# Performance work log

Hardware: AMD Instinct MI355X
Metric: run time of the kernel (lower is better)

## Reference

```python
import jax, jax.numpy as jnp
import numpy as np

N_LEAVES = 4096
NF = N_LEAVES            # one-hot leaf feature dim
NN = 2 * N_LEAVES - 1    # nodes in binary backbone tree
HID = 512
T_MIN, T_MAX = 0.0, 1.0  # time_grid endpoints


def _belief_prop(node_sample, ch0, ch1, parent):
    """Postorder c/d recursion then preorder correction, as in node_embedding_site_backbone.
    Node ids are topologically ordered (children < parent), so postorder = 0..NN-1."""
    is_leaf = node_sample >= 0
    leaf_d = jax.nn.one_hot(jnp.clip(node_sample, 0), NF, dtype=jnp.float32)
    c0 = jnp.zeros((NN,), jnp.float32)
    d0 = jnp.zeros((NN, NF), jnp.float32)

    def post(carry, u):
        c, d = carry
        cc = c[ch0[u]] + c[ch1[u]]
        dd = d[ch0[u]] + d[ch1[u]]
        cu = 1.0 / (3.0 - cc)
        du = cu * dd
        cu = jnp.where(is_leaf[u], 0.0, cu)
        du = jnp.where(is_leaf[u], leaf_d[u], du)
        return (c.at[u].set(cu), d.at[u].set(du)), None

    (c, d), _ = jax.lax.scan(post, (c0, d0), jnp.arange(NN))
    root = NN - 1

    def pre(d, u):
        du = jnp.where(u == root, d[u], c[u] * d[parent[u]] + d[u])
        return d.at[u].set(du), None

    d, _ = jax.lax.scan(pre, d, jnp.arange(NN - 1, -1, -1))
    return d


def _gcn_layer(x, neigh, W, b):
    # neighbor-list GCN: mean over {self} U valid neighbors, then linear
    n = x.shape[0]
    safe = jnp.where(neigh < 0, n, neigh)  # -1 -> extra zero row
    x_ext = jnp.concatenate([x, jnp.zeros((1, x.shape[1]), x.dtype)], axis=0)
    deg = 1.0 + jnp.sum(neigh >= 0, axis=1).astype(x.dtype)
    agg = (x + x_ext[safe].sum(axis=1)) / deg[:, None]
    return agg @ W + b


def setup_inputs():
    rng = np.random.default_rng(0)
    ch0 = -np.ones(NN, np.int64)
    ch1 = -np.ones(NN, np.int64)
    parent = -np.ones(NN, np.int64)
    avail = list(range(N_LEAVES))
    for u in range(N_LEAVES, NN):  # random binary coalescent topology
        a = avail.pop(int(rng.integers(len(avail))))
        b = avail.pop(int(rng.integers(len(avail))))
        ch0[u], ch1[u] = a, b
        parent[a] = u
        parent[b] = u
        avail.append(u)
    root = NN - 1
    node_sample = np.where(np.arange(NN) < N_LEAVES, np.arange(NN), -1).astype(np.int64)
    neigh = -np.ones((NN + 1, 3), np.int64)
    for u in range(NN):
        if u == root:
            neigh[u] = [ch0[u], ch1[u], -1]
        else:
            neigh[u] = [parent[u], ch0[u], ch1[u]]
    branch_child = np.arange(NN, dtype=np.int64)
    is_root = (branch_child == root).astype(np.float32)

    key = jax.random.key(0)
    ks = jax.random.split(key, 8)
    w = lambda k, s: jax.random.normal(k, s, jnp.float32) * 0.02
    E = 4 * HID + 2
    return {
        "node_sample": jnp.asarray(node_sample),
        "ch0": jnp.asarray(ch0),
        "ch1": jnp.asarray(ch1),
        "parent": jnp.asarray(parent),
        "neigh": jnp.asarray(neigh),
        "branch_child": jnp.asarray(branch_child),
        "current_focal_leaf": 7,
        "time_value": jax.random.uniform(ks[0], (NN,), jnp.float32),
        "is_root": jnp.asarray(is_root),
        "W_gnn1": w(ks[1], (NF, HID)), "b_gnn1": jnp.zeros((HID,), jnp.float32),
        "W_gnn2": w(ks[2], (HID, HID)), "b_gnn2": jnp.zeros((HID,), jnp.float32),
        "W_h1": w(ks[3], (E, HID)), "b_h1": jnp.zeros((HID,), jnp.float32),
        "W_h2": w(ks[4], (HID, HID)), "b_h2": jnp.zeros((HID,), jnp.float32),
        "W_h3": w(ks[5], (HID, 1)), "b_h3": jnp.zeros((1,), jnp.float32),
    }


def reference(node_sample, ch0, ch1, parent, neigh, branch_child, current_focal_leaf,
              time_value, is_root, W_gnn1, b_gnn1, W_gnn2, b_gnn2,
              W_h1, b_h1, W_h2, b_h2, W_h3, b_h3):
    d = _belief_prop(node_sample, ch0, ch1, parent)                  # (NN, NF)
    focal_feat = jax.nn.one_hot(current_focal_leaf, NF, dtype=jnp.float32)
    x = jnp.concatenate([d, focal_feat[None, :]], axis=0)            # (NN+1, NF)

    h = jax.nn.relu(_gcn_layer(x, neigh, W_gnn1, b_gnn1))
    emb = _gcn_layer(h, neigh, W_gnn2, b_gnn2)                       # (NN+1, HID)

    h_focal = emb[NN]                                                # appended focal node
    h_tgt = emb[branch_child]                                        # (A, HID)
    h_f = jnp.broadcast_to(h_focal[None, :], h_tgt.shape)
    t_norm = (time_value - T_MIN) / (T_MAX - T_MIN + 1e-8)
    ef = jnp.concatenate([h_f, h_tgt, jnp.abs(h_f - h_tgt), h_f * h_tgt,
                          t_norm[:, None], is_root[:, None]], axis=-1)  # (A, 4*HID+2)

    z = jax.nn.elu(ef @ W_h1 + b_h1)
    z = jax.nn.elu(z @ W_h2 + b_h2)
    logits = (z @ W_h3 + b_h3)[:, 0]
    probs = jax.nn.softmax(logits, axis=0)
    return logits, probs, ef, emb, focal_feat
```

## Files before the change

### kernel.cpp

```cpp
#include <hip/hip_runtime.h>
#include <hip/hip_bf16.h>
#include <math.h>

#define NNODES 8191
#define ROOT   8190
#define NROWS  8192
#define FOCALR 8191
#define NLEAF  4096
#define HID    512
#define EDIM   2050

#define OUT_LOGITS 0
#define OUT_PROBS  8191
#define OUT_EF     16382
#define OUT_EMB    16807932
#define OUT_FOCAL  21002236

typedef float  f32x4 __attribute__((ext_vector_type(4)));
typedef float  f32x2 __attribute__((ext_vector_type(2)));
typedef float  floatx4 __attribute__((ext_vector_type(4)));
typedef short  short8 __attribute__((ext_vector_type(8)));
typedef unsigned short u16;
typedef unsigned short u16x8 __attribute__((ext_vector_type(8)));
typedef unsigned short u16x4 __attribute__((ext_vector_type(4)));

__device__ __forceinline__ f32x4 ldg4(const float* p) { return *(const f32x4*)p; }
__device__ __forceinline__ f32x2 ldg2(const float* p) { return *(const f32x2*)p; }
__device__ __forceinline__ void stg4(float* p, f32x4 v) { *(f32x4*)p = v; }

__device__ __forceinline__ void st_row(float* p, f32x4 v0, f32x4 v1) {
    asm volatile("global_store_dwordx4 %0, %1, off sc0 sc1\n\t"
                 "global_store_dwordx4 %0, %2, off offset:1024 sc0 sc1"
                 :: "v"(p), "v"(v0), "v"(v1) : "memory");
}
__device__ __forceinline__ void st_flag_ordered(float* p, float v) {
    asm volatile("s_waitcnt vmcnt(0)\n\tglobal_store_dword %0, %1, off sc0 sc1"
                 :: "v"(p), "v"(v) : "memory");
}
__device__ __forceinline__ void spin1(const float* pc, float& cv) {
    for (;;) {
        asm volatile("global_load_dword %0, %1, off sc0 sc1\n\ts_waitcnt vmcnt(0)"
                     : "=&v"(cv) : "v"(pc) : "memory");
        if (cv > 0.0f) break;
        __builtin_amdgcn_s_sleep(1);
    }
}
__device__ __forceinline__ void spin2(const float* pa, const float* pb,
                                      float& va, float& vb) {
    for (;;) {
        asm volatile("global_load_dword %0, %2, off sc0 sc1\n\t"
                     "global_load_dword %1, %3, off sc0 sc1\n\t"
                     "s_waitcnt vmcnt(0)"
                     : "=&v"(va), "=&v"(vb) : "v"(pa), "v"(pb) : "memory");
        if (va > 0.0f && vb > 0.0f) break;
        __builtin_amdgcn_s_sleep(1);
    }
}
__device__ __forceinline__ void spin3(const float* pa, const float* pb,
                                      const float* pc, float& va, float& vb, float& vc) {
    for (;;) {
        asm volatile("global_load_dword %0, %3, off sc0 sc1\n\t"
                     "global_load_dword %1, %4, off sc0 sc1\n\t"
                     "global_load_dword %2, %5, off sc0 sc1\n\t"
                     "s_waitcnt vmcnt(0)"
                     : "=&v"(va), "=&v"(vb), "=&v"(vc)
                     : "v"(pa), "v"(pb), "v"(pc) : "memory");
        if (va > 0.0f && vb > 0.0f && vc > 0.0f) break;
        __builtin_amdgcn_s_sleep(1);
    }
}
__device__ __forceinline__ void spin4(const float* p0, const float* p1,
                                      const float* p2, const float* p3,
                                      float& v0, float& v1, float& v2, float& v3) {
    for (;;) {
        asm volatile("global_load_dword %0, %4, off sc0 sc1\n\t"
                     "global_load_dword %1, %5, off sc0 sc1\n\t"
                     "global_load_dword %2, %6, off sc0 sc1\n\t"
                     "global_load_dword %3, %7, off sc0 sc1\n\t"
                     "s_waitcnt vmcnt(0)"
                     : "=&v"(v0), "=&v"(v1), "=&v"(v2), "=&v"(v3)
                     : "v"(p0), "v"(p1), "v"(p2), "v"(p3) : "memory");
        if (v0 > 0.0f && v1 > 0.0f && v2 > 0.0f && v3 > 0.0f) break;
        __builtin_amdgcn_s_sleep(1);
    }
}
__device__ __forceinline__ void rows1_cv(const float* p, f32x4& a0, f32x4& a1) {
    asm volatile("global_load_dwordx4 %0, %2, off sc0 sc1\n\t"
                 "global_load_dwordx4 %1, %2, off offset:1024 sc0 sc1\n\t"
                 "s_waitcnt vmcnt(0)"
                 : "=&v"(a0), "=&v"(a1) : "v"(p) : "memory");
}
__device__ __forceinline__ void rows2_cv(const float* p0, const float* p1,
                                         f32x4& a0, f32x4& a1, f32x4& b0, f32x4& b1) {
    asm volatile("global_load_dwordx4 %0, %4, off sc0 sc1\n\t"
                 "global_load_dwordx4 %1, %4, off offset:1024 sc0 sc1\n\t"
                 "global_load_dwordx4 %2, %5, off sc0 sc1\n\t"
                 "global_load_dwordx4 %3, %5, off offset:1024 sc0 sc1\n\t"
                 "s_waitcnt vmcnt(0)"
                 : "=&v"(a0), "=&v"(a1), "=&v"(b0), "=&v"(b1)
                 : "v"(p0), "v"(p1) : "memory");
}
__device__ __forceinline__ void rows3_cv(const float* p0, const float* p1,
                                         const float* p2,
                                         f32x4& a0, f32x4& a1, f32x4& b0, f32x4& b1,
                                         f32x4& c0, f32x4& c1) {
    asm volatile("global_load_dwordx4 %0, %6, off sc0 sc1\n\t"
                 "global_load_dwordx4 %1, %6, off offset:1024 sc0 sc1\n\t"
                 "global_load_dwordx4 %2, %7, off sc0 sc1\n\t"
                 "global_load_dwordx4 %3, %7, off offset:1024 sc0 sc1\n\t"
                 "global_load_dwordx4 %4, %8, off sc0 sc1\n\t"
                 "global_load_dwordx4 %5, %8, off offset:1024 sc0 sc1\n\t"
                 "s_waitcnt vmcnt(0)"
                 : "=&v"(a0), "=&v"(a1), "=&v"(b0), "=&v"(b1), "=&v"(c0), "=&v"(c1)
                 : "v"(p0), "v"(p1), "v"(p2) : "memory");
}
__device__ __forceinline__ void rows4_cv(const float* p0, const float* p1,
                                         const float* p2, const float* p3,
                                         f32x4& a0, f32x4& a1, f32x4& b0, f32x4& b1,
                                         f32x4& c0, f32x4& c1, f32x4& d0, f32x4& d1) {
    asm volatile("global_load_dwordx4 %0, %8, off sc0 sc1\n\t"
                 "global_load_dwordx4 %1, %8, off offset:1024 sc0 sc1\n\t"
                 "global_load_dwordx4 %2, %9, off sc0 sc1\n\t"
                 "global_load_dwordx4 %3, %9, off offset:1024 sc0 sc1\n\t"
                 "global_load_dwordx4 %4, %10, off sc0 sc1\n\t"
                 "global_load_dwordx4 %5, %10, off offset:1024 sc0 sc1\n\t"
                 "global_load_dwordx4 %6, %11, off sc0 sc1\n\t"
                 "global_load_dwordx4 %7, %11, off offset:1024 sc0 sc1\n\t"
                 "s_waitcnt vmcnt(0)"
                 : "=&v"(a0), "=&v"(a1), "=&v"(b0), "=&v"(b1),
                   "=&v"(c0), "=&v"(c1), "=&v"(d0), "=&v"(d1)
                 : "v"(p0), "v"(p1), "v"(p2), "v"(p3) : "memory");
}
__device__ __forceinline__ f32x4 fma4(f32x4 s, float cv, f32x4 pv) { return s + cv * pv; }

__device__ __forceinline__ u16 f2bf(float x) {
    union { float f; unsigned u; } u; u.f = x;
    unsigned r = u.u + 0x7fffu + ((u.u >> 16) & 1u);
    return (u16)(r >> 16);
}
__device__ __forceinline__ float b2f(u16 h) {
    union { unsigned u; float f; } x; x.u = ((unsigned)h) << 16; return x.f;
}

__global__ void focal_kernel(const int* __restrict__ cfl, float* __restrict__ outf) {
    int i = blockIdx.x * 256 + threadIdx.x;
    if (i < NLEAF) outf[i] = (i == cfl[0]) ? 1.0f : 0.0f;
}

__global__ __launch_bounds__(256) void transpose3_kernel(const float* __restrict__ W2,
                                                         const float* __restrict__ Wh2,
                                                         const float* __restrict__ Wh1,
                                                         u16* __restrict__ wte,
                                                         u16* __restrict__ wt2,
                                                         u16* __restrict__ WTz1) {
    __shared__ float tile[32][33];
    int sec = blockIdx.y >> 4, kt = blockIdx.y & 15;
    int tx = threadIdx.x & 31, ty = threadIdx.x >> 5;
    int n0 = blockIdx.x * 32, k0 = kt * 32;
    const float* src = (sec == 0) ? W2 : (sec == 1) ? Wh2 : (Wh1 + (long)1024 * HID);
    u16* dst = (sec == 0) ? wte : (sec == 1) ? wt2 : WTz1;
    int ld = (sec == 2) ? 1024 : 512;
    int koff = (sec == 2) ? 512 : 0;
#pragma unroll
    for (int i = 0; i < 4; i++)
        tile[ty + i * 8][tx] = src[(long)(k0 + ty + i * 8) * HID + n0 + tx];
    __syncthreads();
#pragma unroll
    for (int i = 0; i < 4; i++)
        dst[(long)(n0 + ty + i * 8) * ld + koff + k0 + tx] = f2bf(tile[tx][ty + i * 8]);
}

__global__ __launch_bounds__(256) void postpre_kernel(const int* __restrict__ ns,
                                                      const int* __restrict__ ch0,
                                                      const int* __restrict__ ch1,
                                                      const int* __restrict__ par,
                                                      const float* __restrict__ W1,
                                                      float* __restrict__ c,
                                                      float* __restrict__ ypost,
                                                      float* __restrict__ y,
                                                      float* __restrict__ flag2) {
    int gtid = blockIdx.x * 256 + threadIdx.x;
    int wave = gtid >> 6, lane = gtid & 63;
    int j0 = lane * 4;

    for (int u = NLEAF + wave; u < NNODES; u += 1024) {
        int a = ch0[u], b = ch1[u];
        int la = ns[a], lb = ns[b];
        const float *ra0, *ra1, *rb0, *rb1;
        int ga0 = -1, ga1 = -1, gb0 = -1, gb1 = -1;
        if (la >= 0) { ra0 = W1 + (long)la * HID; ra1 = ra0; }
        else {
            int x0 = ch0[a], x1 = ch1[a];
            int n0 = ns[x0], n1 = ns[x1];
            if (n0 >= 0) ra0 = W1 + (long)n0 * HID;
            else { ra0 = ypost + (long)x0 * HID; ga0 = x0; }
            if (n1 >= 0) ra1 = W1 + (long)n1 * HID;
            else { ra1 = ypost + (long)x1 * HID; ga1 = x1; }
        }
        if (lb >= 0) { rb0 = W1 + (long)lb * HID; rb1 = rb0; }
        else {
            int x0 = ch0[b], x1 = ch1[b];
            int n0 = ns[x0], n1 = ns[x1];
            if (n0 >= 0) rb0 = W1 + (long)n0 * HID;
            else { rb0 = ypost + (long)x0 * HID; gb0 = x0; }
            if (n1 >= 0) rb1 = W1 + (long)n1 * HID;
            else { rb1 = ypost + (long)x1 * HID; gb1 = x1; }
        }
        float ca0 = 0.f, ca1 = 0.f, cb0 = 0.f, cb1 = 0.f;
        if ((ga0 | ga1 | gb0 | gb1) >= 0) {
            int w0 = ga0 >= 0 ? ga0 : ga1 >= 0 ? ga1 : gb0 >= 0 ? gb0 : gb1;
            float s0, s1, s2, s3;
            spin4(c + (ga0 >= 0 ? ga0 : w0), c + (ga1 >= 0 ? ga1 : w0),
                  c + (gb0 >= 0 ? gb0 : w0), c + (gb1 >= 0 ? gb1 : w0),
                  s0, s1, s2, s3);
            if (ga0 >= 0) ca0 = s0;
            if (ga1 >= 0) ca1 = s1;
            if (gb0 >= 0) cb0 = s2;
            if (gb1 >= 0) cb1 = s3;
        }
        f32x4 qa00, qa01, qa10, qa11, qb00, qb01, qb10, qb11;
        rows4_cv(ra0 + j0, ra1 + j0, rb0 + j0, rb1 + j0,
                 qa00, qa01, qa10, qa11, qb00, qb01, qb10, qb11);
        f32x4 A0, A1, B0, B1; float cA, cB;
        if (la >= 0) { cA = 0.0f; A0 = qa00; A1 = qa01; }
        else {
            cA = 1.0f / (3.0f - (ca0 + ca1));
            A0 = (qa00 + qa10) * cA; A1 = (qa01 + qa11) * cA;
        }
        if (lb >= 0) { cB = 0.0f; B0 = qb00; B1 = qb01; }
        else {
            cB = 1.0f / (3.0f - (cb0 + cb1));
            B0 = (qb00 + qb10) * cB; B1 = (qb01 + qb11) * cB;
        }
        float cu = 1.0f / (3.0f - (cA + cB));
        st_row(ypost + (long)u * HID + j0, (A0 + B0) * cu, (A1 + B1) * cu);
        if (lane == 0) st_flag_ordered(&c[u], cu);
    }

    for (int u = ROOT - wave; u >= NLEAF; u -= 1024) {
        float* dst = y + (long)u * HID + j0;
        if (u == ROOT) {
            float cr;
            spin1(c + ROOT, cr);
            f32x4 s0, s1;
            rows1_cv(ypost + (long)ROOT * HID + j0, s0, s1);
            st_row(dst, s0, s1);
        } else {
            int p = par[u];
            if (p == ROOT) {
                float cr, cu;
                spin2(c + ROOT, c + u, cr, cu);
                f32x4 s0, s1, r0, r1;
                rows2_cv(ypost + (long)u * HID + j0, ypost + (long)ROOT * HID + j0,
                         s0, s1, r0, r1);
                st_row(dst, fma4(s0, cu, r0), fma4(s1, cu, r1));
            } else {
                int gp = par[p];
                float f2, cu, cp;
                spin3(flag2 + gp, c + u, c + p, f2, cu, cp);
                f32x4 s0, s1, pp0, pp1, gg0, gg1;
                rows3_cv(ypost + (long)u * HID + j0, ypost + (long)p * HID + j0,
                         y + (long)gp * HID + j0, s0, s1, pp0, pp1, gg0, gg1);
                f32x4 yp0 = fma4(pp0, cp, gg0);
                f32x4 yp1 = fma4(pp1, cp, gg1);
                st_row(dst, fma4(s0, cu, yp0), fma4(s1, cu, yp1));
            }
        }
        if (lane == 0) st_flag_ordered(&flag2[u], 1.0f);
    }
}

__global__ __launch_bounds__(256) void zprep_kernel(const float* __restrict__ Wh1,
                                                    const float* __restrict__ emb,
                                                    u16* __restrict__ WTz1) {
    __shared__ float tB[32][33];
    __shared__ float tD[32][33];
    const float* hf = emb + (long)FOCALR * HID;
    int tx = threadIdx.x & 31, ty = threadIdx.x >> 5;
    int n0 = blockIdx.x * 32, k0 = blockIdx.y * 32;
#pragma unroll
    for (int i = 0; i < 4; i++) {
        tB[ty + i * 8][tx] = Wh1[(long)(512 + k0 + ty + i * 8) * HID + n0 + tx];
        tD[ty + i * 8][tx] = Wh1[(long)(1536 + k0 + ty + i * 8) * HID + n0 + tx];
    }
    __syncthreads();
#pragma unroll
    for (int i = 0; i < 4; i++) {
        float hfk = hf[k0 + tx];
        WTz1[(long)(n0 + ty + i * 8) * 1024 + k0 + tx] =
            f2bf(tB[tx][ty + i * 8] + hfk * tD[tx][ty + i * 8]);
    }
}

__global__ __launch_bounds__(256) void bvec_part_kernel(const float* __restrict__ Wh1,
                                                        const float* __restrict__ emb,
                                                        float* __restrict__ part) {
    const float* hf = emb + (long)FOCALR * HID;
    int kc = blockIdx.x;
    int t = threadIdx.x;
    float s0 = 0.0f, s1 = 0.0f;
#pragma unroll 4
    for (int k = kc * 64; k < kc * 64 + 64; k++) {
        float h = hf[k];
        s0 += h * Wh1[(long)k * HID + t];
        s1 += h * Wh1[(long)k * HID + 256 + t];
    }
    part[kc * 512 + t] = s0;
    part[kc * 512 + 256 + t] = s1;
}
__global__ __launch_bounds__(256) void bvec_sum_kernel(const float* __restrict__ part,
                                                       const float* __restrict__ bh1,
                                                       float* __restrict__ bprime) {
    int n = blockIdx.x * 256 + threadIdx.x;
    float s = bh1[n];
#pragma unroll
    for (int i = 0; i < 8; i++) s += part[i * 512 + n];
    bprime[n] = s;
}

template <int RELU, int BIAS, int OBF, int REDIR>
__global__ __launch_bounds__(128) void gcn_agg_kernel(const float* __restrict__ xin,
                                                      const int* __restrict__ neigh,
                                                      const float* __restrict__ bias,
                                                      const int* __restrict__ ns,
                                                      const int* __restrict__ cfl,
                                                      const float* __restrict__ W1,
                                                      float* __restrict__ xoutf,
                                                      u16* __restrict__ xoutb) {
    int u = blockIdx.x;
    int t = threadIdx.x;
    int n0 = neigh[u * 3 + 0], n1 = neigh[u * 3 + 1], n2 = neigh[u * 3 + 2];
    float deg = 1.0f + (n0 >= 0) + (n1 >= 0) + (n2 >= 0);
    auto rowp = [&](int v) -> const float* {
        if (!REDIR) return xin + (long)v * HID;
        if (v == FOCALR) return W1 + (long)cfl[0] * HID;
        int nv = ns[v];
        return (nv >= 0) ? (W1 + (long)nv * HID) : (xin + (long)v * HID);
    };
    f32x4 s = ldg4(rowp(u) + t * 4);
    if (n0 >= 0) s += ldg4(rowp(n0) + t * 4);
    if (n1 >= 0) s += ldg4(rowp(n1) + t * 4);
    if (n2 >= 0) s += ldg4(rowp(n2) + t * 4);
    s *= (1.0f / deg);
    if (BIAS) s += ldg4(bias + t * 4);
    if (RELU) { s.x = fmaxf(s.x, 0.f); s.y = fmaxf(s.y, 0.f); s.z = fmaxf(s.z, 0.f); s.w = fmaxf(s.w, 0.f); }
    if (OBF) {
        u16x4 h; h[0] = f2bf(s.x); h[1] = f2bf(s.y); h[2] = f2bf(s.z); h[3] = f2bf(s.w);
        *(u16x4*)(xoutb + (long)u * HID + t * 4) = h;
    } else {
        stg4(xoutf + (long)u * HID + t * 4, s);
    }
}

__device__ __forceinline__ int sw_idx(int row, int kc8) {
    return (row * 8 + (kc8 ^ (row & 7))) * 8;
}

template <int ACT, int AGEN>
__global__ __launch_bounds__(256, 3) void gemm_v5(const u16* __restrict__ Abf,
                                                  const u16* __restrict__ WT,
                                                  const float* __restrict__ bias,
                                                  const int* __restrict__ bc,
                                                  const float* __restrict__ tv,
                                                  const float* __restrict__ isr,
                                                  const float* __restrict__ Wtail,
                                                  float* __restrict__ Cf,
                                                  u16* __restrict__ Cbf,
                                                  int M, int K) {
    __shared__ u16 As[2][64 * 64];
    __shared__ u16 Ws[2][128 * 64];
    const int tid = threadIdx.x, lane = tid & 63;
    const int wm = (tid >> 6) >> 1, wn = (tid >> 6) & 1;
    const int bm = blockIdx.y * 64, bn = blockIdx.x * 128;
    const int kq = lane >> 4, lr = lane & 15;
    const int srow = tid >> 3, schunk = tid & 7;
    const int nk = K >> 6;
    floatx4 acc[2][4] = {};

    int btc[2];
    if (AGEN) {
#pragma unroll
        for (int i = 0; i < 2; i++) {
            int gr = bm + srow + i * 32;
            btc[i] = bc[gr < M ? gr : 0];
        }
    }

    u16x8 pf_hf, pf_a[2], pf_b[4];

    auto prefetch = [&](int kk) {
        if (AGEN) {
            int cb = (kk & 7) * 64 + schunk * 8;
            pf_hf = *(const u16x8*)(Abf + (long)FOCALR * HID + cb);
#pragma unroll
            for (int i = 0; i < 2; i++)
                pf_a[i] = *(const u16x8*)(Abf + (long)btc[i] * HID + cb);
        } else {
            long kof = (long)(kk * 64 + schunk * 8);
#pragma unroll
            for (int i = 0; i < 2; i++) {
                int gr = bm + srow + i * 32;
                if (gr < M) pf_a[i] = *(const u16x8*)(Abf + (long)gr * K + kof);
                else        pf_a[i] = (u16x8){0,0,0,0,0,0,0,0};
            }
        }
#pragma unroll
        for (int i = 0; i < 4; i++)
            pf_b[i] = *(const u16x8*)(WT + (long)(bn + srow + i * 32) * K + kk * 64 + schunk * 8);
    };

    auto commit = [&](int kk, int buf) {
        if (AGEN) {
            int sec = kk >> 3;
#pragma unroll
            for (int i = 0; i < 2; i++) {
                u16x8 v;
                if (sec == 0) v = pf_a[i];
                else {
#pragma unroll
                    for (int q = 0; q < 8; q++) v[q] = f2bf(fabsf(b2f(pf_hf[q]) - b2f(pf_a[i][q])));
                }
                if (bm + srow + i * 32 >= M) v = (u16x8){0,0,0,0,0,0,0,0};
                *(u16x8*)&As[buf][sw_idx(srow + i * 32, schunk)] = v;
            }
        } else {
#pragma unroll
            for (int i = 0; i < 2; i++)
                *(u16x8*)&As[buf][sw_idx(srow + i * 32, schunk)] = pf_a[i];
        }
#pragma unroll
        for (int i = 0; i < 4; i++)
            *(u16x8*)&Ws[buf][sw_idx(srow + i * 32, schunk)] = pf_b[i];
    };

    prefetch(0);
    commit(0, 0);
    __syncthreads();

    for (int kk = 0; kk < nk; kk++) {
        int cur = kk & 1;
        bool more = (kk + 1) < nk;
        if (more) prefetch(kk + 1);
#pragma unroll
        for (int kc = 0; kc < 2; kc++) {
            short8 af[2], bf8[4];
#pragma unroll
            for (int t2 = 0; t2 < 2; t2++)
                af[t2]  = *(short8*)&As[cur][sw_idx(wm * 32 + t2 * 16 + lr, kc * 4 + kq)];
#pragma unroll
            for (int t2 = 0; t2 < 4; t2++)
                bf8[t2] = *(short8*)&Ws[cur][sw_idx(wn * 64 + t2 * 16 + lr, kc * 4 + kq)];
#pragma unroll
            for (int i2 = 0; i2 < 2; i2++)
#pragma unroll
                for (int j = 0; j < 4; j++)
                    acc[i2][j] = __builtin_amdgcn_mfma_f32_16x16x32_bf16(af[i2], bf8[j], acc[i2][j], 0, 0, 0);
        }
        if (more) {
            __syncthreads();
            commit(kk + 1, cur ^ 1);
            __syncthreads();
        }
    }

#pragma unroll
    for (int i = 0; i < 2; i++) {
        int row0 = bm + wm * 32 + i * 16 + kq * 4;
#pragma unroll
        for (int j = 0; j < 4; j++) {
            int col = bn + wn * 64 + j * 16 + lr;
            float bv = bias[col];
            float t0 = 0.f, t1 = 0.f;
            if (AGEN) { t0 = Wtail[col]; t1 = Wtail[512 + col]; }
#pragma unroll
            for (int r = 0; r < 4; r++) {
                int gr = row0 + r;
                if (gr < M) {
                    float v = acc[i][j][r] + bv;
                    if (AGEN) v += tv[gr] * t0 + isr[gr] * t1;
                    if (ACT == 2) v = (v > 0.0f) ? v : (expf(v) - 1.0f);
                    if (Cf)  Cf[(long)gr * HID + col] = v;
                    if (Cbf) Cbf[(long)gr * HID + col] = f2bf(v);
                }
            }
        }
    }
}

__global__ __launch_bounds__(256) void ef_kernel(const float* __restrict__ emb,
                                                 const int* __restrict__ bc,
                                                 const float* __restrict__ tv,
                                                 const float* __restrict__ isr,
                                                 float* __restrict__ ef) {
    int u = blockIdx.x;
    int t = threadIdx.x;
    const float* hf = emb + (long)FOCALR * HID;
    const float* ht = emb + (long)bc[u] * HID;
    f32x2 f = ldg2(hf + 2 * t);
    f32x2 h = ldg2(ht + 2 * t);
    float* row = ef + (long)u * EDIM;
    *(f32x2*)(row + 2 * t) = f;
    *(f32x2*)(row + 512 + 2 * t) = h;
    f32x2 d; d[0] = fabsf(f[0] - h[0]); d[1] = fabsf(f[1] - h[1]);
    *(f32x2*)(row + 1024 + 2 * t) = d;
    f32x2 p; p[0] = f[0] * h[0]; p[1] = f[1] * h[1];
    *(f32x2*)(row + 1536 + 2 * t) = p;
    if (t == 0) {
        row[2048] = tv[u];
        row[2049] = isr[u];
    }
}

__global__ __launch_bounds__(256) void logits_kernel(const float* __restrict__ z2,
                                                     const float* __restrict__ W3,
                                                     const float* __restrict__ b3,
                                                     float* __restrict__ out) {
    int wv = threadIdx.x >> 6, lane = threadIdx.x & 63;
    int row = blockIdx.x * 4 + wv;
    if (row >= NNODES) return;
    const float* zr = z2 + (long)row * HID;
    float s = 0.0f;
#pragma unroll
    for (int j = 0; j < 8; j++) s += zr[lane * 8 + j] * W3[lane * 8 + j];
    for (int o = 32; o; o >>= 1) s += __shfl_down(s, o);
    if (lane == 0) out[row] = s + b3[0];
}

__global__ __launch_bounds__(1024) void softmax_kernel(const float* __restrict__ lg,
                                                       float* __restrict__ probs) {
    __shared__ float red[16];
    __shared__ float gmax_s, gsum_s;
    int t = threadIdx.x, wid = t >> 6, lane = t & 63;
    float m = -3.4e38f;
    for (int i = t; i < NNODES; i += 1024) m = fmaxf(m, lg[i]);
    for (int o = 32; o; o >>= 1) m = fmaxf(m, __shfl_down(m, o));
    if (lane == 0) red[wid] = m;
    __syncthreads();
    if (t == 0) {
        float g = red[0];
        for (int i = 1; i < 16; i++) g = fmaxf(g, red[i]);
        gmax_s = g;
    }
    __syncthreads();
    float gmax = gmax_s;
    float s = 0.0f;
    for (int i = t; i < NNODES; i += 1024) s += expf(lg[i] - gmax);
    for (int o = 32; o; o >>= 1) s += __shfl_down(s, o);
    if (lane == 0) red[wid] = s;
    __syncthreads();
    if (t == 0) {
        float g = 0.0f;
        for (int i = 0; i < 16; i++) g += red[i];
        gsum_s = g;
    }
    __syncthreads();
    float inv = 1.0f / gsum_s;
    for (int i = t; i < NNODES; i += 1024) probs[i] = expf(lg[i] - gmax) * inv;
}

extern "C" void kernel_launch(void* const* d_in, const int* in_sizes, int n_in,
                              void* d_out, int out_size, void* d_ws, size_t ws_size,
                              hipStream_t stream) {
    const int*   ns    = (const int*)d_in[0];
    const int*   ch0   = (const int*)d_in[1];
    const int*   ch1   = (const int*)d_in[2];
    const int*   par   = (const int*)d_in[3];
    const int*   neigh = (const int*)d_in[4];
    const int*   bc    = (const int*)d_in[5];
    const int*   cfl   = (const int*)d_in[6];
    const float* tv    = (const float*)d_in[7];
    const float* isr   = (const float*)d_in[8];
    const float* W1    = (const float*)d_in[9];
    const float* b1    = (const float*)d_in[10];
    const float* W2    = (const float*)d_in[11];
    const float* b2    = (const float*)d_in[12];
    const float* Wh1   = (const float*)d_in[13];
    const float* bh1   = (const float*)d_in[14];
    const float* Wh2   = (const float*)d_in[15];
    const float* bh2   = (const float*)d_in[16];
    const float* Wh3   = (const float*)d_in[17];
    const float* bh3   = (const float*)d_in[18];

    float* out = (float*)d_out;
    float* out_logits = out + OUT_LOGITS;
    float* out_probs  = out + OUT_PROBS;
    float* out_ef     = out + OUT_EF;
    float* out_emb    = out + OUT_EMB;
    float* out_focal  = out + OUT_FOCAL;

    const size_t MB = 1024 * 1024;
    char* ws = (char*)d_ws;
    float* c      = (float*)(ws);
    float* flag2  = (float*)(ws + 40960);
    float* buf0   = (float*)(ws + 81920);
    float* buf1   = (float*)(ws + 81920 + 16 * MB);
    float* buf2   = (float*)(ws + 81920 + 32 * MB);
    u16*   wte    = (u16*)  (ws + 81920 + 48 * MB);
    u16*   wt2    = (u16*)  (ws + 81920 + 48 * MB + 512 * 1024);
    u16*   wtz1   = (u16*)  (ws + 81920 + 49 * MB);
    float* bprime = (float*)(ws + 81920 + 50 * MB);
    float* bpart  = (float*)(ws + 81920 + 50 * MB + 4096);

    float* ypost  = buf0;
    float* z2f    = buf0;
    float* y      = buf1;
    u16*   a2_bf  = (u16*)buf1;
    u16*   emb_bf = (u16*)((char*)buf1 + 8 * MB);
    float* h      = buf2;
    u16*   z1_bf  = (u16*)buf2;

    focal_kernel<<<dim3(16), dim3(256), 0, stream>>>(cfl, out_focal);
    transpose3_kernel<<<dim3(16, 48), dim3(256), 0, stream>>>(W2, Wh2, Wh1, wte, wt2, wtz1);
    postpre_kernel<<<dim3(256), dim3(256), 0, stream>>>(ns, ch0, ch1, par, W1, c, ypost,
                                                        y, flag2);
    gcn_agg_kernel<1, 1, 0, 1><<<dim3(NROWS), dim3(128), 0, stream>>>(y, neigh, b1, ns, cfl,
                                                                      W1, h, nullptr);
    gcn_agg_kernel<0, 0, 1, 0><<<dim3(NROWS), dim3(128), 0, stream>>>(h, neigh, b1, ns, cfl,
                                                                      W1, nullptr, a2_bf);
    gemm_v5<0, 0><<<dim3(4, 128), dim3(256), 0, stream>>>(a2_bf, wte, b2, nullptr, nullptr,
                                                          nullptr, nullptr, out_emb, emb_bf,
                                                          NROWS, HID);
    ef_kernel<<<dim3(NNODES), dim3(256), 0, stream>>>(out_emb, bc, tv, isr, out_ef);
    zprep_kernel<<<dim3(16, 16), dim3(256), 0, stream>>>(Wh1, out_emb, wtz1);
    bvec_part_kernel<<<dim3(8), dim3(256), 0, stream>>>(Wh1, out_emb, bpart);
    bvec_sum_kernel<<<dim3(2), dim3(256), 0, stream>>>(bpart, bh1, bprime);
    gemm_v5<2, 1><<<dim3(4, 128), dim3(256), 0, stream>>>(emb_bf, wtz1, bprime, bc, tv, isr,
                                                          Wh1 + (long)2048 * HID, nullptr,
                                                          z1_bf, NNODES, 1024);
    gemm_v5<2, 0><<<dim3(4, 128), dim3(256), 0, stream>>>(z1_bf, wt2, bh2, nullptr, nullptr,
                                                          nullptr, nullptr, z2f, nullptr,
                                                          NNODES, HID);
    logits_kernel<<<dim3(2048), dim3(256), 0, stream>>>(z2f, Wh3, bh3, out_logits);
    softmax_kernel<<<dim3(1), dim3(1024), 0, stream>>>(out_logits, out_probs);
}
```

Baseline: 303.3 us.

## Merge setup kernels, fuse logits into last GEMM, store hidden in bf16

Several independent launches are merged into block-index-dispatched kernels. The focal one-hot, weight transposes, belief propagation and output/bias initialisation go into one stage1 kernel. The ef construction, Wh1 folding and bias-vector partial sums go into one emb_fan kernel. The logits dot product moves into the final GEMM epilogue as a shuffle reduction plus atomicAdd, so the z2 float buffer and the logits kernel are no longer needed. The first GCN layer output is now stored as bf16, which halves the traffic of the intermediate but lowers its precision and adds atomic contention on the logits.

Result: faster. 279.1 us (-8.0%).

```diff
diff --git a/kernel.cpp b/kernel.cpp
--- a/kernel.cpp
+++ b/kernel.cpp
@@ -142,162 +142,200 @@
     union { unsigned u; float f; } x; x.u = ((unsigned)h) << 16; return x.f;
 }
 
-__global__ void focal_kernel(const int* __restrict__ cfl, float* __restrict__ outf) {
-    int i = blockIdx.x * 256 + threadIdx.x;
-    if (i < NLEAF) outf[i] = (i == cfl[0]) ? 1.0f : 0.0f;
-}
-
-__global__ __launch_bounds__(256) void transpose3_kernel(const float* __restrict__ W2,
-                                                         const float* __restrict__ Wh2,
-                                                         const float* __restrict__ Wh1,
-                                                         u16* __restrict__ wte,
-                                                         u16* __restrict__ wt2,
-                                                         u16* __restrict__ WTz1) {
+__global__ __launch_bounds__(256) void stage1_kernel(const int* __restrict__ ns,
+                                                     const int* __restrict__ ch0,
+                                                     const int* __restrict__ ch1,
+                                                     const int* __restrict__ par,
+                                                     const float* __restrict__ W1,
+                                                     float* __restrict__ c,
+                                                     float* __restrict__ ypost,
+                                                     float* __restrict__ y,
+                                                     float* __restrict__ flag2,
+                                                     const float* __restrict__ W2,
+                                                     const float* __restrict__ Wh2,
+                                                     const float* __restrict__ Wh1,
+                                                     u16* __restrict__ wte,
+                                                     u16* __restrict__ wt2,
+                                                     u16* __restrict__ WTz1,
+                                                     const int* __restrict__ cfl,
+                                                     float* __restrict__ outf,
+                                                     const float* __restrict__ bh1,
+                                                     float* __restrict__ bprime,
+                                                     const float* __restrict__ bh3,
+                                                     float* __restrict__ outlog) {
     __shared__ float tile[32][33];
-    int sec = blockIdx.y >> 4, kt = blockIdx.y & 15;
-    int tx = threadIdx.x & 31, ty = threadIdx.x >> 5;
-    int n0 = blockIdx.x * 32, k0 = kt * 32;
-    const float* src = (sec == 0) ? W2 : (sec == 1) ? Wh2 : (Wh1 + (long)1024 * HID);
-    u16* dst = (sec == 0) ? wte : (sec == 1) ? wt2 : WTz1;
-    int ld = (sec == 2) ? 1024 : 512;
-    int koff = (sec == 2) ? 512 : 0;
-#pragma unroll
-    for (int i = 0; i < 4; i++)
-        tile[ty + i * 8][tx] = src[(long)(k0 + ty + i * 8) * HID + n0 + tx];
-    __syncthreads();
-#pragma unroll
-    for (int i = 0; i < 4; i++)
-        dst[(long)(n0 + ty + i * 8) * ld + koff + k0 + tx] = f2bf(tile[tx][ty + i * 8]);
-}
-
-__global__ __launch_bounds__(256) void postpre_kernel(const int* __restrict__ ns,
-                                                      const int* __restrict__ ch0,
-                                                      const int* __restrict__ ch1,
-                                                      const int* __restrict__ par,
-                                                      const float* __restrict__ W1,
-                                                      float* __restrict__ c,
-                                                      float* __restrict__ ypost,
-                                                      float* __restrict__ y,
-                                                      float* __restrict__ flag2) {
-    int gtid = blockIdx.x * 256 + threadIdx.x;
-    int wave = gtid >> 6, lane = gtid & 63;
-    int j0 = lane * 4;
-
-    for (int u = NLEAF + wave; u < NNODES; u += 1024) {
-        int a = ch0[u], b = ch1[u];
-        int la = ns[a], lb = ns[b];
-        const float *ra0, *ra1, *rb0, *rb1;
-        int ga0 = -1, ga1 = -1, gb0 = -1, gb1 = -1;
-        if (la >= 0) { ra0 = W1 + (long)la * HID; ra1 = ra0; }
-        else {
-            int x0 = ch0[a], x1 = ch1[a];
-            int n0 = ns[x0], n1 = ns[x1];
-            if (n0 >= 0) ra0 = W1 + (long)n0 * HID;
-            else { ra0 = ypost + (long)x0 * HID; ga0 = x0; }
-            if (n1 >= 0) ra1 = W1 + (long)n1 * HID;
-            else { ra1 = ypost + (long)x1 * HID; ga1 = x1; }
-        }
-        if (lb >= 0) { rb0 = W1 + (long)lb * HID; rb1 = rb0; }
-        else {
-            int x0 = ch0[b], x1 = ch1[b];
-            int n0 = ns[x0], n1 = ns[x1];
-            if (n0 >= 0) rb0 = W1 + (long)n0 * HID;
-            else { rb0 = ypost + (long)x0 * HID; gb0 = x0; }
-            if (n1 >= 0) rb1 = W1 + (long)n1 * HID;
-            else { rb1 = ypost + (long)x1 * HID; gb1 = x1; }
-        }
-        float ca0 = 0.f, ca1 = 0.f, cb0 = 0.f, cb1 = 0.f;
-        if ((ga0 | ga1 | gb0 | gb1) >= 0) {
-            int w0 = ga0 >= 0 ? ga0 : ga1 >= 0 ? ga1 : gb0 >= 0 ? gb0 : gb1;
-            float s0, s1, s2, s3;
-            spin4(c + (ga0 >= 0 ? ga0 : w0), c + (ga1 >= 0 ? ga1 : w0),
-                  c + (gb0 >= 0 ? gb0 : w0), c + (gb1 >= 0 ? gb1 : w0),
-                  s0, s1, s2, s3);
-            if (ga0 >= 0) ca0 = s0;
-            if (ga1 >= 0) ca1 = s1;
-            if (gb0 >= 0) cb0 = s2;
-            if (gb1 >= 0) cb1 = s3;
-        }
-        f32x4 qa00, qa01, qa10, qa11, qb00, qb01, qb10, qb11;
-        rows4_cv(ra0 + j0, ra1 + j0, rb0 + j0, rb1 + j0,
-                 qa00, qa01, qa10, qa11, qb00, qb01, qb10, qb11);
-        f32x4 A0, A1, B0, B1; float cA, cB;
-        if (la >= 0) { cA = 0.0f; A0 = qa00; A1 = qa01; }
-        else {
-            cA = 1.0f / (3.0f - (ca0 + ca1));
-            A0 = (qa00 + qa10) * cA; A1 = (qa01 + qa11) * cA;
-        }
-        if (lb >= 0) { cB = 0.0f; B0 = qb00; B1 = qb01; }
-        else {
-            cB = 1.0f / (3.0f - (cb0 + cb1));
-            B0 = (qb00 + qb10) * cB; B1 = (qb01 + qb11) * cB;
-        }
-        float cu = 1.0f / (3.0f - (cA + cB));
-        st_row(ypost + (long)u * HID + j0, (A0 + B0) * cu, (A1 + B1) * cu);
-        if (lane == 0) st_flag_ordered(&c[u], cu);
-    }
-
-    for (int u = ROOT - wave; u >= NLEAF; u -= 1024) {
-        float* dst = y + (long)u * HID + j0;
-        if (u == ROOT) {
-            float cr;
-            spin1(c + ROOT, cr);
-            f32x4 s0, s1;
-            rows1_cv(ypost + (long)ROOT * HID + j0, s0, s1);
-            st_row(dst, s0, s1);
-        } else {
-            int p = par[u];
-            if (p == ROOT) {
-                float cr, cu;
-                spin2(c + ROOT, c + u, cr, cu);
-                f32x4 s0, s1, r0, r1;
-                rows2_cv(ypost + (long)u * HID + j0, ypost + (long)ROOT * HID + j0,
-                         s0, s1, r0, r1);
-                st_row(dst, fma4(s0, cu, r0), fma4(s1, cu, r1));
+    int bid = blockIdx.x, tid = threadIdx.x;
+
+    if (bid < 256) {
+        int gtid = bid * 256 + tid;
+        int wave = gtid >> 6, lane = gtid & 63;
+        int j0 = lane * 4;
+
+        for (int u = NLEAF + wave; u < NNODES; u += 1024) {
+            int a = ch0[u], b = ch1[u];
+            int la = ns[a], lb = ns[b];
+            const float *ra0, *ra1, *rb0, *rb1;
+            int ga0 = -1, ga1 = -1, gb0 = -1, gb1 = -1;
+            if (la >= 0) { ra0 = W1 + (long)la * HID; ra1 = ra0; }
+            else {
+                int x0 = ch0[a], x1 = ch1[a];
+                int n0 = ns[x0], n1 = ns[x1];
+                if (n0 >= 0) ra0 = W1 + (long)n0 * HID;
+                else { ra0 = ypost + (long)x0 * HID; ga0 = x0; }
+                if (n1 >= 0) ra1 = W1 + (long)n1 * HID;
+                else { ra1 = ypost + (long)x1 * HID; ga1 = x1; }
+            }
+            if (lb >= 0) { rb0 = W1 + (long)lb * HID; rb1 = rb0; }
+            else {
+                int x0 = ch0[b], x1 = ch1[b];
+                int n0 = ns[x0], n1 = ns[x1];
+                if (n0 >= 0) rb0 = W1 + (long)n0 * HID;
+                else { rb0 = ypost + (long)x0 * HID; gb0 = x0; }
+                if (n1 >= 0) rb1 = W1 + (long)n1 * HID;
+                else { rb1 = ypost + (long)x1 * HID; gb1 = x1; }
+            }
+            float ca0 = 0.f, ca1 = 0.f, cb0 = 0.f, cb1 = 0.f;
+            if ((ga0 | ga1 | gb0 | gb1) >= 0) {
+                int w0 = ga0 >= 0 ? ga0 : ga1 >= 0 ? ga1 : gb0 >= 0 ? gb0 : gb1;
+                float s0, s1, s2, s3;
+                spin4(c + (ga0 >= 0 ? ga0 : w0), c + (ga1 >= 0 ? ga1 : w0),
+                      c + (gb0 >= 0 ? gb0 : w0), c + (gb1 >= 0 ? gb1 : w0),
+                      s0, s1, s2, s3);
+                if (ga0 >= 0) ca0 = s0;
+                if (ga1 >= 0) ca1 = s1;
+                if (gb0 >= 0) cb0 = s2;
+                if (gb1 >= 0) cb1 = s3;
+            }
+            f32x4 qa00, qa01, qa10, qa11, qb00, qb01, qb10, qb11;
+            rows4_cv(ra0 + j0, ra1 + j0, rb0 + j0, rb1 + j0,
+                     qa00, qa01, qa10, qa11, qb00, qb01, qb10, qb11);
+            f32x4 A0, A1, B0, B1; float cA, cB;
+            if (la >= 0) { cA = 0.0f; A0 = qa00; A1 = qa01; }
+            else {
+                cA = 1.0f / (3.0f - (ca0 + ca1));
+                A0 = (qa00 + qa10) * cA; A1 = (qa01 + qa11) * cA;
+            }
+            if (lb >= 0) { cB = 0.0f; B0 = qb00; B1 = qb01; }
+            else {
+                cB = 1.0f / (3.0f - (cb0 + cb1));
+                B0 = (qb00 + qb10) * cB; B1 = (qb01 + qb11) * cB;
+            }
+            float cu = 1.0f / (3.0f - (cA + cB));
+            st_row(ypost + (long)u * HID + j0, (A0 + B0) * cu, (A1 + B1) * cu);
+            if (lane == 0) st_flag_ordered(&c[u], cu);
+        }
+
+        for (int u = ROOT - wave; u >= NLEAF; u -= 1024) {
+            float* dst = y + (long)u * HID + j0;
+            if (u == ROOT) {
+                float cr;
+                spin1(c + ROOT, cr);
+                f32x4 s0, s1;
+                rows1_cv(ypost + (long)ROOT * HID + j0, s0, s1);
+                st_row(dst, s0, s1);
             } else {
-                int gp = par[p];
-                float f2, cu, cp;
-                spin3(flag2 + gp, c + u, c + p, f2, cu, cp);
-                f32x4 s0, s1, pp0, pp1, gg0, gg1;
-                rows3_cv(ypost + (long)u * HID + j0, ypost + (long)p * HID + j0,
-                         y + (long)gp * HID + j0, s0, s1, pp0, pp1, gg0, gg1);
-                f32x4 yp0 = fma4(pp0, cp, gg0);
-                f32x4 yp1 = fma4(pp1, cp, gg1);
-                st_row(dst, fma4(s0, cu, yp0), fma4(s1, cu, yp1));
-            }
-        }
-        if (lane == 0) st_flag_ordered(&flag2[u], 1.0f);
-    }
-}
-
-__global__ __launch_bounds__(256) void zprep_kernel(const float* __restrict__ Wh1,
-                                                    const float* __restrict__ emb,
-                                                    u16* __restrict__ WTz1) {
+                int p = par[u];
+                if (p == ROOT) {
+                    float cr, cu;
+                    spin2(c + ROOT, c + u, cr, cu);
+                    f32x4 s0, s1, r0, r1;
+                    rows2_cv(ypost + (long)u * HID + j0, ypost + (long)ROOT * HID + j0,
+                             s0, s1, r0, r1);
+                    st_row(dst, fma4(s0, cu, r0), fma4(s1, cu, r1));
+                } else {
+                    int gp = par[p];
+                    float f2, cu, cp;
+                    spin3(flag2 + gp, c + u, c + p, f2, cu, cp);
+                    f32x4 s0, s1, pp0, pp1, gg0, gg1;
+                    rows3_cv(ypost + (long)u * HID + j0, ypost + (long)p * HID + j0,
+                             y + (long)gp * HID + j0, s0, s1, pp0, pp1, gg0, gg1);
+                    f32x4 yp0 = fma4(pp0, cp, gg0);
+                    f32x4 yp1 = fma4(pp1, cp, gg1);
+                    st_row(dst, fma4(s0, cu, yp0), fma4(s1, cu, yp1));
+                }
+            }
+            if (lane == 0) st_flag_ordered(&flag2[u], 1.0f);
+        }
+        return;
+    }
+
+    if (bid < 1024) {
+        int t = bid - 256;
+        int bx = t & 15, by = t >> 4;
+        int sec = by >> 4, kt = by & 15;
+        int tx = tid & 31, ty = tid >> 5;
+        int n0 = bx * 32, k0 = kt * 32;
+        const float* src = (sec == 0) ? W2 : (sec == 1) ? Wh2 : (Wh1 + (long)1024 * HID);
+        u16* dst = (sec == 0) ? wte : (sec == 1) ? wt2 : WTz1;
+        int ld = (sec == 2) ? 1024 : 512;
+        int koff = (sec == 2) ? 512 : 0;
+#pragma unroll
+        for (int i = 0; i < 4; i++)
+            tile[ty + i * 8][tx] = src[(long)(k0 + ty + i * 8) * HID + n0 + tx];
+        __syncthreads();
+#pragma unroll
+        for (int i = 0; i < 4; i++)
+            dst[(long)(n0 + ty + i * 8) * ld + koff + k0 + tx] = f2bf(tile[tx][ty + i * 8]);
+        return;
+    }
+
+    int cf = cfl[0];
+    for (int i = tid; i < NLEAF; i += 256) outf[i] = (i == cf) ? 1.0f : 0.0f;
+    float b3v = bh3[0];
+    for (int i = tid; i < NNODES; i += 256) outlog[i] = b3v;
+    for (int i = tid; i < 512; i += 256) bprime[i] = bh1[i];
+}
+
+__global__ __launch_bounds__(256) void emb_fan_kernel(const float* __restrict__ emb,
+                                                      const int* __restrict__ bc,
+                                                      const float* __restrict__ tv,
+                                                      const float* __restrict__ isr,
+                                                      float* __restrict__ ef,
+                                                      const float* __restrict__ Wh1,
+                                                      u16* __restrict__ WTz1,
+                                                      float* __restrict__ bprime) {
     __shared__ float tB[32][33];
     __shared__ float tD[32][33];
+    int bid = blockIdx.x, t = threadIdx.x;
     const float* hf = emb + (long)FOCALR * HID;
-    int tx = threadIdx.x & 31, ty = threadIdx.x >> 5;
-    int n0 = blockIdx.x * 32, k0 = blockIdx.y * 32;
-#pragma unroll
-    for (int i = 0; i < 4; i++) {
-        tB[ty + i * 8][tx] = Wh1[(long)(512 + k0 + ty + i * 8) * HID + n0 + tx];
-        tD[ty + i * 8][tx] = Wh1[(long)(1536 + k0 + ty + i * 8) * HID + n0 + tx];
-    }
-    __syncthreads();
-#pragma unroll
-    for (int i = 0; i < 4; i++) {
-        float hfk = hf[k0 + tx];
-        WTz1[(long)(n0 + ty + i * 8) * 1024 + k0 + tx] =
-            f2bf(tB[tx][ty + i * 8] + hfk * tD[tx][ty + i * 8]);
-    }
-}
-
-__global__ __launch_bounds__(256) void bvec_part_kernel(const float* __restrict__ Wh1,
-                                                        const float* __restrict__ emb,
-                                                        float* __restrict__ part) {
-    const float* hf = emb + (long)FOCALR * HID;
-    int kc = blockIdx.x;
-    int t = threadIdx.x;
+
+    if (bid < NNODES) {
+        int u = bid;
+        const float* ht = emb + (long)bc[u] * HID;
+        f32x2 f = ldg2(hf + 2 * t);
+        f32x2 h = ldg2(ht + 2 * t);
+        float* row = ef + (long)u * EDIM;
+        *(f32x2*)(row + 2 * t) = f;
+        *(f32x2*)(row + 512 + 2 * t) = h;
+        f32x2 d; d[0] = fabsf(f[0] - h[0]); d[1] = fabsf(f[1] - h[1]);
+        *(f32x2*)(row + 1024 + 2 * t) = d;
+        f32x2 p; p[0] = f[0] * h[0]; p[1] = f[1] * h[1];
+        *(f32x2*)(row + 1536 + 2 * t) = p;
+        if (t == 0) {
+            row[2048] = tv[u];
+            row[2049] = isr[u];
+        }
+        return;
+    }
+    if (bid < NNODES + 256) {
+        int q = bid - NNODES;
+        int tx = t & 31, ty = t >> 5;
+        int n0 = (q & 15) * 32, k0 = (q >> 4) * 32;
+#pragma unroll
+        for (int i = 0; i < 4; i++) {
+            tB[ty + i * 8][tx] = Wh1[(long)(512 + k0 + ty + i * 8) * HID + n0 + tx];
+            tD[ty + i * 8][tx] = Wh1[(long)(1536 + k0 + ty + i * 8) * HID + n0 + tx];
+        }
+        __syncthreads();
+#pragma unroll
+        for (int i = 0; i < 4; i++) {
+            float hfk = hf[k0 + tx];
+            WTz1[(long)(n0 + ty + i * 8) * 1024 + k0 + tx] =
+                f2bf(tB[tx][ty + i * 8] + hfk * tD[tx][ty + i * 8]);
+        }
+        return;
+    }
+    int kc = bid - NNODES - 256;
     float s0 = 0.0f, s1 = 0.0f;
 #pragma unroll 4
     for (int k = kc * 64; k < kc * 64 + 64; k++) {
@@ -305,21 +343,13 @@
         s0 += h * Wh1[(long)k * HID + t];
         s1 += h * Wh1[(long)k * HID + 256 + t];
     }
-    part[kc * 512 + t] = s0;
-    part[kc * 512 + 256 + t] = s1;
-}
-__global__ __launch_bounds__(256) void bvec_sum_kernel(const float* __restrict__ part,
-                                                       const float* __restrict__ bh1,
-                                                       float* __restrict__ bprime) {
-    int n = blockIdx.x * 256 + threadIdx.x;
-    float s = bh1[n];
-#pragma unroll
-    for (int i = 0; i < 8; i++) s += part[i * 512 + n];
-    bprime[n] = s;
-}
-
-template <int RELU, int BIAS, int OBF, int REDIR>
-__global__ __launch_bounds__(128) void gcn_agg_kernel(const float* __restrict__ xin,
+    atomicAdd(bprime + t, s0);
+    atomicAdd(bprime + 256 + t, s1);
+}
+
+template <int RELU, int BIAS, int OBF, int REDIR, int INBF>
+__global__ __launch_bounds__(128) void gcn_agg_kernel(const float* __restrict__ xinf,
+                                                      const u16* __restrict__ xinb,
                                                       const int* __restrict__ neigh,
                                                       const float* __restrict__ bias,
                                                       const int* __restrict__ ns,
@@ -331,16 +361,29 @@
     int t = threadIdx.x;
     int n0 = neigh[u * 3 + 0], n1 = neigh[u * 3 + 1], n2 = neigh[u * 3 + 2];
     float deg = 1.0f + (n0 >= 0) + (n1 >= 0) + (n2 >= 0);
-    auto rowp = [&](int v) -> const float* {
-        if (!REDIR) return xin + (long)v * HID;
-        if (v == FOCALR) return W1 + (long)cfl[0] * HID;
-        int nv = ns[v];
-        return (nv >= 0) ? (W1 + (long)nv * HID) : (xin + (long)v * HID);
-    };
-    f32x4 s = ldg4(rowp(u) + t * 4);
-    if (n0 >= 0) s += ldg4(rowp(n0) + t * 4);
-    if (n1 >= 0) s += ldg4(rowp(n1) + t * 4);
-    if (n2 >= 0) s += ldg4(rowp(n2) + t * 4);
+    f32x4 s;
+    if (INBF) {
+        auto rdbf = [&](int v) -> f32x4 {
+            u16x4 h4 = *(const u16x4*)(xinb + (long)v * HID + t * 4);
+            f32x4 r; r.x = b2f(h4[0]); r.y = b2f(h4[1]); r.z = b2f(h4[2]); r.w = b2f(h4[3]);
+            return r;
+        };
+        s = rdbf(u);
+        if (n0 >= 0) s += rdbf(n0);
+        if (n1 >= 0) s += rdbf(n1);
+        if (n2 >= 0) s += rdbf(n2);
+    } else {
+        auto rowp = [&](int v) -> const float* {
+            if (!REDIR) return xinf + (long)v * HID;
+            if (v == FOCALR) return W1 + (long)cfl[0] * HID;
+            int nv = ns[v];
+            return (nv >= 0) ? (W1 + (long)nv * HID) : (xinf + (long)v * HID);
+        };
+        s = ldg4(rowp(u) + t * 4);
+        if (n0 >= 0) s += ldg4(rowp(n0) + t * 4);
+        if (n1 >= 0) s += ldg4(rowp(n1) + t * 4);
+        if (n2 >= 0) s += ldg4(rowp(n2) + t * 4);
+    }
     s *= (1.0f / deg);
     if (BIAS) s += ldg4(bias + t * 4);
     if (RELU) { s.x = fmaxf(s.x, 0.f); s.y = fmaxf(s.y, 0.f); s.z = fmaxf(s.z, 0.f); s.w = fmaxf(s.w, 0.f); }
@@ -356,7 +399,7 @@
     return (row * 8 + (kc8 ^ (row & 7))) * 8;
 }
 
-template <int ACT, int AGEN>
+template <int ACT, int AGEN, int LOG>
 __global__ __launch_bounds__(256, 3) void gemm_v5(const u16* __restrict__ Abf,
                                                   const u16* __restrict__ WT,
                                                   const float* __restrict__ bias,
@@ -366,7 +409,9 @@
                                                   const float* __restrict__ Wtail,
                                                   float* __restrict__ Cf,
                                                   u16* __restrict__ Cbf,
-                                                  int M, int K) {
+                                                  int M, int K,
+                                                  const float* __restrict__ W3,
+                                                  float* __restrict__ outlog) {
     __shared__ u16 As[2][64 * 64];
     __shared__ u16 Ws[2][128 * 64];
     const int tid = threadIdx.x, lane = tid & 63;
@@ -463,6 +508,12 @@
         }
     }
 
+    float lsum[2][4] = {};
+    float w3v[4] = {};
+    if (LOG) {
+#pragma unroll
+        for (int j = 0; j < 4; j++) w3v[j] = W3[bn + wn * 64 + j * 16 + lr];
+    }
 #pragma unroll
     for (int i = 0; i < 2; i++) {
         int row0 = bm + wm * 32 + i * 16 + kq * 4;
@@ -479,51 +530,31 @@
                     float v = acc[i][j][r] + bv;
                     if (AGEN) v += tv[gr] * t0 + isr[gr] * t1;
                     if (ACT == 2) v = (v > 0.0f) ? v : (expf(v) - 1.0f);
+                    if (LOG) lsum[i][r] += v * w3v[j];
                     if (Cf)  Cf[(long)gr * HID + col] = v;
                     if (Cbf) Cbf[(long)gr * HID + col] = f2bf(v);
                 }
             }
         }
     }
-}
-
-__global__ __launch_bounds__(256) void ef_kernel(const float* __restrict__ emb,
-                                                 const int* __restrict__ bc,
-                                                 const float* __restrict__ tv,
-                                                 const float* __restrict__ isr,
-                                                 float* __restrict__ ef) {
-    int u = blockIdx.x;
-    int t = threadIdx.x;
-    const float* hf = emb + (long)FOCALR * HID;
-    const float* ht = emb + (long)bc[u] * HID;
-    f32x2 f = ldg2(hf + 2 * t);
-    f32x2 h = ldg2(ht + 2 * t);
-    float* row = ef + (long)u * EDIM;
-    *(f32x2*)(row + 2 * t) = f;
-    *(f32x2*)(row + 512 + 2 * t) = h;
-    f32x2 d; d[0] = fabsf(f[0] - h[0]); d[1] = fabsf(f[1] - h[1]);
-    *(f32x2*)(row + 1024 + 2 * t) = d;
-    f32x2 p; p[0] = f[0] * h[0]; p[1] = f[1] * h[1];
-    *(f32x2*)(row + 1536 + 2 * t) = p;
-    if (t == 0) {
-        row[2048] = tv[u];
-        row[2049] = isr[u];
-    }
-}
-
-__global__ __launch_bounds__(256) void logits_kernel(const float* __restrict__ z2,
-                                                     const float* __restrict__ W3,
-                                                     const float* __restrict__ b3,
-                                                     float* __restrict__ out) {
-    int wv = threadIdx.x >> 6, lane = threadIdx.x & 63;
-    int row = blockIdx.x * 4 + wv;
-    if (row >= NNODES) return;
-    const float* zr = z2 + (long)row * HID;
-    float s = 0.0f;
-#pragma unroll
-    for (int j = 0; j < 8; j++) s += zr[lane * 8 + j] * W3[lane * 8 + j];
-    for (int o = 32; o; o >>= 1) s += __shfl_down(s, o);
-    if (lane == 0) out[row] = s + b3[0];
+    if (LOG) {
+#pragma unroll
+        for (int i = 0; i < 2; i++) {
+            int row0 = bm + wm * 32 + i * 16 + kq * 4;
+#pragma unroll
+            for (int r = 0; r < 4; r++) {
+                float s = lsum[i][r];
+                s += __shfl_xor(s, 1);
+                s += __shfl_xor(s, 2);
+                s += __shfl_xor(s, 4);
+                s += __shfl_xor(s, 8);
+                if (lr == 0) {
+                    int gr = row0 + r;
+                    if (gr < M) atomicAdd(outlog + gr, s);
+                }
+            }
+        }
+    }
 }
 
 __global__ __launch_bounds__(1024) void softmax_kernel(const float* __restrict__ lg,
@@ -599,37 +630,32 @@
     u16*   wt2    = (u16*)  (ws + 81920 + 48 * MB + 512 * 1024);
     u16*   wtz1   = (u16*)  (ws + 81920 + 49 * MB);
     float* bprime = (float*)(ws + 81920 + 50 * MB);
-    float* bpart  = (float*)(ws + 81920 + 50 * MB + 4096);
 
     float* ypost  = buf0;
-    float* z2f    = buf0;
     float* y      = buf1;
     u16*   a2_bf  = (u16*)buf1;
     u16*   emb_bf = (u16*)((char*)buf1 + 8 * MB);
-    float* h      = buf2;
+    u16*   h_bf   = (u16*)buf2;
     u16*   z1_bf  = (u16*)buf2;
 
-    focal_kernel<<<dim3(16), dim3(256), 0, stream>>>(cfl, out_focal);
-    transpose3_kernel<<<dim3(16, 48), dim3(256), 0, stream>>>(W2, Wh2, Wh1, wte, wt2, wtz1);
-    postpre_kernel<<<dim3(256), dim3(256), 0, stream>>>(ns, ch0, ch1, par, W1, c, ypost,
-                                                        y, flag2);
-    gcn_agg_kernel<1, 1, 0, 1><<<dim3(NROWS), dim3(128), 0, stream>>>(y, neigh, b1, ns, cfl,
-                                                                      W1, h, nullptr);
-    gcn_agg_kernel<0, 0, 1, 0><<<dim3(NROWS), dim3(128), 0, stream>>>(h, neigh, b1, ns, cfl,
-                                                                      W1, nullptr, a2_bf);
-    gemm_v5<0, 0><<<dim3(4, 128), dim3(256), 0, stream>>>(a2_bf, wte, b2, nullptr, nullptr,
-                                                          nullptr, nullptr, out_emb, emb_bf,
-                                                          NROWS, HID);
-    ef_kernel<<<dim3(NNODES), dim3(256), 0, stream>>>(out_emb, bc, tv, isr, out_ef);
-    zprep_kernel<<<dim3(16, 16), dim3(256), 0, stream>>>(Wh1, out_emb, wtz1);
-    bvec_part_kernel<<<dim3(8), dim3(256), 0, stream>>>(Wh1, out_emb, bpart);
-    bvec_sum_kernel<<<dim3(2), dim3(256), 0, stream>>>(bpart, bh1, bprime);
-    gemm_v5<2, 1><<<dim3(4, 128), dim3(256), 0, stream>>>(emb_bf, wtz1, bprime, bc, tv, isr,
-                                                          Wh1 + (long)2048 * HID, nullptr,
-                                                          z1_bf, NNODES, 1024);
-    gemm_v5<2, 0><<<dim3(4, 128), dim3(256), 0, stream>>>(z1_bf, wt2, bh2, nullptr, nullptr,
-                                                          nullptr, nullptr, z2f, nullptr,
-                                                          NNODES, HID);
-    logits_kernel<<<dim3(2048), dim3(256), 0, stream>>>(z2f, Wh3, bh3, out_logits);
+    stage1_kernel<<<dim3(1025), dim3(256), 0, stream>>>(ns, ch0, ch1, par, W1, c, ypost,
+                                                        y, flag2, W2, Wh2, Wh1, wte, wt2,
+                                                        wtz1, cfl, out_focal, bh1, bprime,
+                                                        bh3, out_logits);
+    gcn_agg_kernel<1, 1, 1, 1, 0><<<dim3(NROWS), dim3(128), 0, stream>>>(
+        y, nullptr, neigh, b1, ns, cfl, W1, nullptr, h_bf);
+    gcn_agg_kernel<0, 0, 1, 0, 1><<<dim3(NROWS), dim3(128), 0, stream>>>(
+        nullptr, h_bf, neigh, b1, ns, cfl, W1, nullptr, a2_bf);
+    gemm_v5<0, 0, 0><<<dim3(4, 128), dim3(256), 0, stream>>>(
+        a2_bf, wte, b2, nullptr, nullptr, nullptr, nullptr, out_emb, emb_bf,
+        NROWS, HID, nullptr, nullptr);
+    emb_fan_kernel<<<dim3(NNODES + 256 + 8), dim3(256), 0, stream>>>(
+        out_emb, bc, tv, isr, out_ef, Wh1, wtz1, bprime);
+    gemm_v5<2, 1, 0><<<dim3(4, 128), dim3(256), 0, stream>>>(
+        emb_bf, wtz1, bprime, bc, tv, isr, Wh1 + (long)2048 * HID, nullptr, z1_bf,
+        NNODES, 1024, nullptr, nullptr);
+    gemm_v5<2, 0, 1><<<dim3(4, 128), dim3(256), 0, stream>>>(
+        z1_bf, wt2, bh2, nullptr, nullptr, nullptr, nullptr, nullptr, nullptr,
+        NNODES, HID, Wh3, out_logits);
     softmax_kernel<<<dim3(1), dim3(1024), 0, stream>>>(out_logits, out_probs);
 }
```
